# Kernel tuning notes

Hardware: AMD Instinct MI355X
Metric: run time of the kernel (lower is better)

The kernel has to match this reference:

```python
import jax, jax.numpy as jnp
import numpy as np

N, D = 500000, 128
Z_SCALE = 1e-3  # keeps exp(sum_i R_i*||Z_i||^2) finite at this N


def setup_inputs() -> dict:
    key = jax.random.key(0)
    kz, kr = jax.random.split(key)
    Z = jax.random.normal(kz, (N, D), dtype=jnp.float32) * Z_SCALE
    R = jax.random.normal(kr, (N,), dtype=jnp.float32)
    return {"Z": Z, "R": R}


def reference(Z, R):
    # Original: sigmaInput = diag(R) * (Z @ Z^T); sum(sigmaInput).
    # diag(R) zeroes every off-diagonal entry, so the sum is exactly
    # sum_i R_i * ||Z_i||^2 -- an O(N*D) weighted row-norm reduction.
    # (Dropout with p=0 is the identity.)
    s = jnp.sum(R * jnp.sum(Z * Z, axis=-1))          # scalar
    lambdaterm = jnp.exp(s)
    logits = 1.0 - jnp.exp(-lambdaterm)               # RelaxedBernoulli logits
    return logits
```

## Files before the change

### kernel.cpp

```cpp
#include <hip/hip_runtime.h>
#include <math.h>


#define NROWS 500000
#define DCOLS 128
#define TOTAL4 (NROWS * (DCOLS / 4))

__global__ void __launch_bounds__(256)
bp_reduce(const float* __restrict__ Z, const float* __restrict__ R,
          float* __restrict__ partial) {
    const float4* __restrict__ Z4 = (const float4*)Z;
    int tid = blockIdx.x * blockDim.x + threadIdx.x;
    int stride = gridDim.x * blockDim.x;

    float acc = 0.0f;
    for (int i = tid; i < TOTAL4; i += stride) {
        float4 v = Z4[i];
        float w = R[i >> 5];
        acc += w * (v.x * v.x + v.y * v.y + v.z * v.z + v.w * v.w);
    }

    #pragma unroll
    for (int off = 32; off > 0; off >>= 1)
        acc += __shfl_down(acc, off, 64);

    __shared__ float smem[4];
    int wave = threadIdx.x >> 6;
    int lane = threadIdx.x & 63;
    if (lane == 0) smem[wave] = acc;
    __syncthreads();

    if (threadIdx.x == 0) {
        float s = smem[0] + smem[1] + smem[2] + smem[3];
        atomicAdd(partial, s);
    }
}

__global__ void bp_finalize(const float* __restrict__ partial,
                            float* __restrict__ out) {
    float s = *partial;
    float lam = expf(s);
    out[0] = 1.0f - expf(-lam);
}

extern "C" void kernel_launch(void* const* d_in, const int* in_sizes, int n_in,
                              void* d_out, int out_size, void* d_ws, size_t ws_size,
                              hipStream_t stream) {
    const float* Z = (const float*)d_in[0];
    const float* R = (const float*)d_in[1];
    float* out = (float*)d_out;
    float* partial = (float*)d_ws;

    hipMemsetAsync(partial, 0, sizeof(float), stream);

    const int block = 256;
    const int grid = 4096;
    bp_reduce<<<grid, block, 0, stream>>>(Z, R, partial);
    bp_finalize<<<1, 1, 0, stream>>>(partial, out);
}
```

Measured before the change: 352.2 us.

## Unroll exact-fit streaming loads and replace atomics with two-stage reduction

```diff
diff --git a/kernel.cpp b/kernel.cpp
--- a/kernel.cpp
+++ b/kernel.cpp
@@ -2,45 +2,77 @@
 #include <math.h>
 
 
-#define NROWS 500000
-#define DCOLS 128
-#define TOTAL4 (NROWS * (DCOLS / 4))
+#define NROWS   500000
+#define DCOLS   128
+#define N4      (NROWS * DCOLS / 4)
+#define BLOCK   256
+#define GRID    2500
+#define NTHREADS (GRID * BLOCK)
+#define OUTER   5
+#define INNER   5
 
-__global__ void __launch_bounds__(256)
+typedef float floatx4 __attribute__((ext_vector_type(4)));
+
+__global__ void __launch_bounds__(BLOCK)
 bp_reduce(const float* __restrict__ Z, const float* __restrict__ R,
           float* __restrict__ partial) {
-    const float4* __restrict__ Z4 = (const float4*)Z;
-    int tid = blockIdx.x * blockDim.x + threadIdx.x;
-    int stride = gridDim.x * blockDim.x;
+    const floatx4* __restrict__ Z4 = (const floatx4*)Z;
+    const int tid = blockIdx.x * BLOCK + threadIdx.x;
 
     float acc = 0.0f;
-    for (int i = tid; i < TOTAL4; i += stride) {
-        float4 v = Z4[i];
-        float w = R[i >> 5];
-        acc += w * (v.x * v.x + v.y * v.y + v.z * v.z + v.w * v.w);
+    int i = tid;
+    #pragma unroll
+    for (int o = 0; o < OUTER; ++o) {
+        floatx4 v[INNER];
+        float   w[INNER];
+        #pragma unroll
+        for (int u = 0; u < INNER; ++u) {
+            const int idx = i + u * NTHREADS;
+            v[u] = __builtin_nontemporal_load(&Z4[idx]);
+            w[u] = R[idx >> 5];
+        }
+        #pragma unroll
+        for (int u = 0; u < INNER; ++u)
+            acc += w[u] * (v[u].x * v[u].x + v[u].y * v[u].y +
+                           v[u].z * v[u].z + v[u].w * v[u].w);
+        i += INNER * NTHREADS;
     }
 
     #pragma unroll
     for (int off = 32; off > 0; off >>= 1)
         acc += __shfl_down(acc, off, 64);
 
-    __shared__ float smem[4];
-    int wave = threadIdx.x >> 6;
-    int lane = threadIdx.x & 63;
+    __shared__ float smem[BLOCK / 64];
+    const int wave = threadIdx.x >> 6;
+    const int lane = threadIdx.x & 63;
+    if (lane == 0) smem[wave] = acc;
+    __syncthreads();
+
+    if (threadIdx.x == 0)
+        partial[blockIdx.x] = smem[0] + smem[1] + smem[2] + smem[3];
+}
+
+__global__ void __launch_bounds__(BLOCK)
+bp_finalize(const float* __restrict__ partial, float* __restrict__ out) {
+    float acc = 0.0f;
+    for (int i = threadIdx.x; i < GRID; i += BLOCK)
+        acc += partial[i];
+
+    #pragma unroll
+    for (int off = 32; off > 0; off >>= 1)
+        acc += __shfl_down(acc, off, 64);
+
+    __shared__ float smem[BLOCK / 64];
+    const int wave = threadIdx.x >> 6;
+    const int lane = threadIdx.x & 63;
     if (lane == 0) smem[wave] = acc;
     __syncthreads();
 
     if (threadIdx.x == 0) {
         float s = smem[0] + smem[1] + smem[2] + smem[3];
-        atomicAdd(partial, s);
+        float lam = expf(s);
+        out[0] = 1.0f - expf(-lam);
     }
-}
-
-__global__ void bp_finalize(const float* __restrict__ partial,
-                            float* __restrict__ out) {
-    float s = *partial;
-    float lam = expf(s);
-    out[0] = 1.0f - expf(-lam);
 }
 
 extern "C" void kernel_launch(void* const* d_in, const int* in_sizes, int n_in,
@@ -51,10 +83,6 @@
     float* out = (float*)d_out;
     float* partial = (float*)d_ws;
 
-    hipMemsetAsync(partial, 0, sizeof(float), stream);
-
-    const int block = 256;
-    const int grid = 4096;
-    bp_reduce<<<grid, block, 0, stream>>>(Z, R, partial);
-    bp_finalize<<<1, 1, 0, stream>>>(partial, out);
+    bp_reduce<<<GRID, BLOCK, 0, stream>>>(Z, R, partial);
+    bp_finalize<<<1, BLOCK, 0, stream>>>(partial, out);
 }
```

Result: faster. 320.0 us (-9.1%).
